# Optimization experiments

Hardware: AMD Instinct MI355X
Metric: run time of the kernel (lower is better)

Reference implementation:

```python
import jax, jax.numpy as jnp
import numpy as np

TOP_K = 2  # num_experts_per_tok


def setup_inputs() -> dict:
    key = jax.random.key(0)
    k1, k2, k3, k4, k5 = jax.random.split(key, 5)
    B, S, D, F, E = 2, 1024, 1024, 2048, 8
    return {
        "x": jax.random.normal(k1, (B, S, D), dtype=jnp.float32),
        "router_kernel_DE": jax.random.normal(k2, (D, E), dtype=jnp.float32) * 0.02,
        "kernel_gating_EDF": jax.random.normal(k3, (E, D, F), dtype=jnp.float32) * 0.02,
        "kernel_up_EDF": jax.random.normal(k4, (E, D, F), dtype=jnp.float32) * 0.02,
        "kernel_down_EFD": jax.random.normal(k5, (E, F, D), dtype=jnp.float32) * 0.02,
    }


def reference(x, router_kernel_DE, kernel_gating_EDF, kernel_up_EDF, kernel_down_EFD):
    E = router_kernel_DE.shape[-1]
    x = x.astype(jnp.float32)
    # --- Router ---
    logits_BSE = jnp.einsum('BSD,DE->BSE', x, router_kernel_DE)
    probs_BSE = jax.nn.softmax(logits_BSE.astype(jnp.float32), axis=-1)
    weights_BSK, indices_BSK = jax.lax.top_k(probs_BSE, TOP_K)
    norm_weights_BSK = jax.nn.softmax(weights_BSK, axis=-1)
    # scatter top-k weights into dense [B,S,E]
    one_hot_BSKE = jax.nn.one_hot(indices_BSK, num_classes=E, dtype=x.dtype)
    full_weights_BSE = jnp.sum(one_hot_BSKE * norm_weights_BSK[..., None], axis=2)
    # --- Dense-over-all-experts MoE forward ---
    gating_BSEF = jnp.einsum('BSD,EDF->BSEF', x, kernel_gating_EDF)
    act_BSEF = jax.nn.silu(gating_BSEF)
    up_BSEF = jnp.einsum('BSD,EDF->BSEF', x, kernel_up_EDF)
    fuse_BSEF = act_BSEF * up_BSEF
    down_BSED = jnp.einsum('BSEF,EFD->BSED', fuse_BSEF, kernel_down_EFD)
    out_BSD = jnp.einsum('BSED,BSE->BSD', down_BSED, full_weights_BSE)
    return out_BSD.astype(jnp.float32)
```

## Files before the change

### kernel.cpp

```cpp
#include <hip/hip_runtime.h>
#include <hip/hip_bf16.h>
#include <stdint.h>

#define T_TOK 2048
#define DIM 1024
#define FDIM 2048
#define NEXP 8
#define NSLOT 4096

typedef short bf16x8 __attribute__((ext_vector_type(8)));
typedef float f32x4 __attribute__((ext_vector_type(4)));

__device__ __forceinline__ unsigned short f2bf(float f) {
  union { float f; unsigned int u; } v; v.f = f;
  unsigned int r = v.u + 0x7FFFu + ((v.u >> 16) & 1u);
  return (unsigned short)(r >> 16);
}

__device__ __forceinline__ void gld_lds16(const void* g, void* l) {
  __builtin_amdgcn_global_load_lds(
      (const __attribute__((address_space(1))) unsigned int*)g,
      (__attribute__((address_space(3))) unsigned int*)l, 16, 0, 0);
}

__global__ void router_kernel(const float* __restrict__ x, const float* __restrict__ rk,
                              int* __restrict__ counts, int* __restrict__ tok_e,
                              float* __restrict__ tok_w) {
  int w = threadIdx.x >> 6, lane = threadIdx.x & 63;
  int t = blockIdx.x * 4 + w;
  float acc[NEXP];
#pragma unroll
  for (int e = 0; e < NEXP; ++e) acc[e] = 0.f;
  const float4* xr = (const float4*)(x + (size_t)t * DIM);
#pragma unroll
  for (int i = 0; i < 4; ++i) {
    float4 xv = xr[i * 64 + lane];
    int d0 = (i * 64 + lane) * 4;
#pragma unroll
    for (int j = 0; j < 4; ++j) {
      const float4* rr = (const float4*)(rk + (size_t)(d0 + j) * NEXP);
      float4 r0 = rr[0], r1 = rr[1];
      float xs = (j == 0) ? xv.x : (j == 1) ? xv.y : (j == 2) ? xv.z : xv.w;
      acc[0] += xs * r0.x; acc[1] += xs * r0.y; acc[2] += xs * r0.z; acc[3] += xs * r0.w;
      acc[4] += xs * r1.x; acc[5] += xs * r1.y; acc[6] += xs * r1.z; acc[7] += xs * r1.w;
    }
  }
#pragma unroll
  for (int off = 32; off > 0; off >>= 1) {
#pragma unroll
    for (int e = 0; e < NEXP; ++e) acc[e] += __shfl_xor(acc[e], off, 64);
  }
  if (lane == 0) {
    float m = acc[0];
    for (int e = 1; e < NEXP; ++e) m = fmaxf(m, acc[e]);
    float p[NEXP], s = 0.f;
    for (int e = 0; e < NEXP; ++e) { p[e] = expf(acc[e] - m); s += p[e]; }
    float inv = 1.f / s;
    for (int e = 0; e < NEXP; ++e) p[e] *= inv;
    int i1 = 0;
    for (int e = 1; e < NEXP; ++e) if (p[e] > p[i1]) i1 = e;
    int i2 = (i1 == 0) ? 1 : 0;
    for (int e = 0; e < NEXP; ++e) if (e != i1 && p[e] > p[i2]) i2 = e;
    float e1 = expf(p[i1]), e2 = expf(p[i2]);
    float winv = 1.f / (e1 + e2);
    tok_e[t * 2] = i1; tok_e[t * 2 + 1] = i2;
    tok_w[t * 2] = e1 * winv; tok_w[t * 2 + 1] = e2 * winv;
    atomicAdd(&counts[i1], 1); atomicAdd(&counts[i2], 1);
  }
}

__global__ void scan_kernel(const int* __restrict__ counts, int* __restrict__ offsets) {
  if (threadIdx.x == 0) {
    int s = 0;
    for (int e = 0; e < NEXP; ++e) { offsets[e] = s; s += counts[e]; }
  }
}

__global__ void assign_kernel(const int* __restrict__ tok_e, const float* __restrict__ tok_w,
                              const int* __restrict__ offsets, int* __restrict__ cursor,
                              int* __restrict__ slot_token, float* __restrict__ slot_weight,
                              int* __restrict__ tok_slot) {
  int t = blockIdx.x * 256 + threadIdx.x;
  if (t >= T_TOK) return;
#pragma unroll
  for (int k = 0; k < 2; ++k) {
    int e = tok_e[t * 2 + k];
    int pos = atomicAdd(&cursor[e], 1);
    int slot = offsets[e] + pos;
    slot_token[slot] = t;
    slot_weight[slot] = tok_w[t * 2 + k];
    tok_slot[t * 2 + k] = slot;
  }
}

__global__ void cvt_x_kernel(const float* __restrict__ x, unsigned short* __restrict__ xb) {
  int i = blockIdx.x * 256 + threadIdx.x;
  const float4* p = (const float4*)x;
  float4 a = p[i * 2], b = p[i * 2 + 1];
  uint4 o;
  o.x = ((unsigned)f2bf(a.y) << 16) | f2bf(a.x);
  o.y = ((unsigned)f2bf(a.w) << 16) | f2bf(a.z);
  o.z = ((unsigned)f2bf(b.y) << 16) | f2bf(b.x);
  o.w = ((unsigned)f2bf(b.w) << 16) | f2bf(b.z);
  ((uint4*)xb)[i] = o;
}

__global__ void transpose_cvt_kernel(const float* __restrict__ in, unsigned short* __restrict__ out,
                                     int R, int C) {
  __shared__ float lds[64][65];
  int e = blockIdx.z;
  size_t base = (size_t)e * (size_t)R * (size_t)C;
  int rb = blockIdx.y * 64, cb = blockIdx.x * 64;
  int tid = threadIdx.x;
  int col4 = (tid & 15) * 4, row = tid >> 4;
#pragma unroll
  for (int it = 0; it < 4; ++it) {
    int r = row + it * 16;
    float4 v = *(const float4*)(in + base + (size_t)(rb + r) * C + cb + col4);
    lds[col4 + 0][r] = v.x; lds[col4 + 1][r] = v.y;
    lds[col4 + 2][r] = v.z; lds[col4 + 3][r] = v.w;
  }
  __syncthreads();
  int r2 = (tid & 31) * 2, c = tid >> 5;
#pragma unroll
  for (int it = 0; it < 8; ++it) {
    int cc = c + it * 8;
    unsigned v = ((unsigned)f2bf(lds[cc][r2 + 1]) << 16) | f2bf(lds[cc][r2]);
    *(unsigned*)(out + base + (size_t)(cb + cc) * R + rb + r2) = v;
  }
}


__global__ __launch_bounds__(256) void gemm_gateup(
    const unsigned short* __restrict__ xb, const unsigned short* __restrict__ wg,
    const unsigned short* __restrict__ wu, const int* __restrict__ counts,
    const int* __restrict__ offsets, const int* __restrict__ slot_token,
    unsigned short* __restrict__ fuse) {
  int e = blockIdx.z;
  int cnt = counts[e];
  int mt = blockIdx.y;
  if (mt * 128 >= cnt) return;
  int off = offsets[e];
  int nt = blockIdx.x;
  __shared__ unsigned short Al[2][128 * 64];
  __shared__ unsigned short Bgl[2][128 * 64];
  __shared__ unsigned short Bul[2][128 * 64];
  int tid = threadIdx.x, w = tid >> 6, lane = tid & 63;
  int w4 = w * 4;
  int csrc = ((lane & 7) ^ (lane >> 3)) * 8;
  const unsigned short* asrc[4];
  const unsigned short* bgsrc[4];
  const unsigned short* busrc[4];
#pragma unroll
  for (int ii = 0; ii < 4; ++ii) {
    int i = w4 + ii;
    int r = i * 8 + (lane >> 3);
    int row = mt * 128 + r;
    int tok = (row < cnt) ? slot_token[off + row] : 0;
    asrc[ii] = xb + (size_t)tok * DIM + csrc;
    size_t frow = (size_t)e * FDIM + (size_t)(nt * 128 + r);
    bgsrc[ii] = wg + frow * DIM + csrc;
    busrc[ii] = wu + frow * DIM + csrc;
  }
  f32x4 accg[4][4] = {};
  f32x4 accu[4][4] = {};
  int wr = (w >> 1) * 64, wc = (w & 1) * 64;
  int swz = (lane & 7) << 3;
  int kof0 = ((lane >> 4) * 8) ^ swz;
  int kof1 = (32 + (lane >> 4) * 8) ^ swz;

  auto stage = [&](int buf, int k0) {
#pragma unroll
    for (int ii = 0; ii < 4; ++ii) {
      int i = w4 + ii;
      gld_lds16(asrc[ii] + k0, &Al[buf][i * 512]);
      gld_lds16(bgsrc[ii] + k0, &Bgl[buf][i * 512]);
      gld_lds16(busrc[ii] + k0, &Bul[buf][i * 512]);
    }
  };
  auto compute = [&](int buf) {
#pragma unroll
    for (int kk = 0; kk < 2; ++kk) {
      int kof = kk ? kof1 : kof0;
      bf16x8 af[4], bg[4], bu[4];
#pragma unroll
      for (int q = 0; q < 4; ++q) {
        af[q] = *(const bf16x8*)&Al[buf][(wr + q * 16 + (lane & 15)) * 64 + kof];
        bg[q] = *(const bf16x8*)&Bgl[buf][(wc + q * 16 + (lane & 15)) * 64 + kof];
        bu[q] = *(const bf16x8*)&Bul[buf][(wc + q * 16 + (lane & 15)) * 64 + kof];
      }
#pragma unroll
      for (int m4 = 0; m4 < 4; ++m4) {
#pragma unroll
        for (int n4 = 0; n4 < 4; ++n4) {
          accg[m4][n4] = __builtin_amdgcn_mfma_f32_16x16x32_bf16(af[m4], bg[n4], accg[m4][n4], 0, 0, 0);
          accu[m4][n4] = __builtin_amdgcn_mfma_f32_16x16x32_bf16(af[m4], bu[n4], accu[m4][n4], 0, 0, 0);
        }
      }
    }
  };

  stage(0, 0);
  __syncthreads();
#pragma unroll
  for (int k0 = 0; k0 < DIM; k0 += 128) {
    stage(1, k0 + 64);
    compute(0);
    __syncthreads();
    if (k0 + 128 < DIM) stage(0, k0 + 128);
    compute(1);
    __syncthreads();
  }

#pragma unroll
  for (int m4 = 0; m4 < 4; ++m4) {
#pragma unroll
    for (int n4 = 0; n4 < 4; ++n4) {
      f32x4 g = accg[m4][n4], u = accu[m4][n4];
#pragma unroll
      for (int j = 0; j < 4; ++j) {
        int r = wr + m4 * 16 + (lane >> 4) * 4 + j;
        int row = mt * 128 + r;
        if (row < cnt) {
          float gv = g[j];
          float val = gv / (1.f + expf(-gv)) * u[j];
          int f = nt * 128 + wc + n4 * 16 + (lane & 15);
          fuse[(size_t)(off + row) * FDIM + f] = f2bf(val);
        }
      }
    }
  }
}

__global__ __launch_bounds__(256) void gemm_down(
    const unsigned short* __restrict__ fuse, const unsigned short* __restrict__ wd,
    const int* __restrict__ counts, const int* __restrict__ offsets,
    const float* __restrict__ slot_weight, float* __restrict__ part) {
  int e = blockIdx.z;
  int cnt = counts[e];
  int mt = blockIdx.y;
  if (mt * 128 >= cnt) return;
  int off = offsets[e];
  int nt = blockIdx.x;
  __shared__ unsigned short Al[2][128 * 64];
  __shared__ unsigned short Bl[2][128 * 64];
  int tid = threadIdx.x, w = tid >> 6, lane = tid & 63;
  int w4 = w * 4;
  int csrc = ((lane & 7) ^ (lane >> 3)) * 8;
  const unsigned short* asrc[4];
  const unsigned short* bsrc[4];
#pragma unroll
  for (int ii = 0; ii < 4; ++ii) {
    int i = w4 + ii;
    int r = i * 8 + (lane >> 3);
    int row = mt * 128 + r;
    int grow = (row < cnt) ? (off + row) : off;
    asrc[ii] = fuse + (size_t)grow * FDIM + csrc;
    size_t drow = (size_t)e * DIM + (size_t)(nt * 128 + r);
    bsrc[ii] = wd + drow * FDIM + csrc;
  }
  f32x4 acc[4][4] = {};
  int wr = (w >> 1) * 64, wc = (w & 1) * 64;
  int swz = (lane & 7) << 3;
  int kof0 = ((lane >> 4) * 8) ^ swz;
  int kof1 = (32 + (lane >> 4) * 8) ^ swz;

  auto stage = [&](int buf, int k0) {
#pragma unroll
    for (int ii = 0; ii < 4; ++ii) {
      int i = w4 + ii;
      gld_lds16(asrc[ii] + k0, &Al[buf][i * 512]);
      gld_lds16(bsrc[ii] + k0, &Bl[buf][i * 512]);
    }
  };
  auto compute = [&](int buf) {
#pragma unroll
    for (int kk = 0; kk < 2; ++kk) {
      int kof = kk ? kof1 : kof0;
      bf16x8 af[4], bfr[4];
#pragma unroll
      for (int q = 0; q < 4; ++q) {
        af[q] = *(const bf16x8*)&Al[buf][(wr + q * 16 + (lane & 15)) * 64 + kof];
        bfr[q] = *(const bf16x8*)&Bl[buf][(wc + q * 16 + (lane & 15)) * 64 + kof];
      }
#pragma unroll
      for (int m4 = 0; m4 < 4; ++m4) {
#pragma unroll
        for (int n4 = 0; n4 < 4; ++n4) {
          acc[m4][n4] = __builtin_amdgcn_mfma_f32_16x16x32_bf16(af[m4], bfr[n4], acc[m4][n4], 0, 0, 0);
        }
      }
    }
  };

  stage(0, 0);
  __syncthreads();
#pragma unroll
  for (int k0 = 0; k0 < FDIM; k0 += 128) {
    stage(1, k0 + 64);
    compute(0);
    __syncthreads();
    if (k0 + 128 < FDIM) stage(0, k0 + 128);
    compute(1);
    __syncthreads();
  }

#pragma unroll
  for (int m4 = 0; m4 < 4; ++m4) {
#pragma unroll
    for (int j = 0; j < 4; ++j) {
      int r = wr + m4 * 16 + (lane >> 4) * 4 + j;
      int row = mt * 128 + r;
      if (row < cnt) {
        float wgt = slot_weight[off + row];
#pragma unroll
        for (int n4 = 0; n4 < 4; ++n4) {
          int d = nt * 128 + wc + n4 * 16 + (lane & 15);
          part[(size_t)(off + row) * DIM + d] = acc[m4][n4][j] * wgt;
        }
      }
    }
  }
}

__global__ void combine_kernel(const float* __restrict__ part, const int* __restrict__ tok_slot,
                               float* __restrict__ out) {
  int i = blockIdx.x * 256 + threadIdx.x;
  int t = i >> 8;
  int c = i & 255;
  int s0 = tok_slot[t * 2], s1 = tok_slot[t * 2 + 1];
  float4 a = ((const float4*)(part + (size_t)s0 * DIM))[c];
  float4 b = ((const float4*)(part + (size_t)s1 * DIM))[c];
  float4 o;
  o.x = a.x + b.x; o.y = a.y + b.y; o.z = a.z + b.z; o.w = a.w + b.w;
  ((float4*)(out + (size_t)t * DIM))[c] = o;
}

extern "C" void kernel_launch(void* const* d_in, const int* in_sizes, int n_in,
                              void* d_out, int out_size, void* d_ws, size_t ws_size,
                              hipStream_t stream) {
  (void)in_sizes; (void)n_in; (void)out_size;
  const float* x    = (const float*)d_in[0];
  const float* rk   = (const float*)d_in[1];
  const float* wg_f = (const float*)d_in[2];
  const float* wu_f = (const float*)d_in[3];
  const float* wd_f = (const float*)d_in[4];
  float* out = (float*)d_out;

  char* ws = (char*)d_ws;
  size_t o_xb   = 0;
  size_t o_wg   = o_xb + (size_t)T_TOK * DIM * 2;
  size_t o_wu   = o_wg + (size_t)NEXP * FDIM * DIM * 2;
  size_t o_wd   = o_wu + (size_t)NEXP * FDIM * DIM * 2;
  size_t o_fuse = o_wd + (size_t)NEXP * DIM * FDIM * 2;
  size_t o_part = o_fuse + (size_t)NSLOT * FDIM * 2;
  size_t o_meta = o_part + (size_t)NSLOT * DIM * 4;
  size_t o_counts = o_meta;
  size_t o_cursor = o_counts + 32;
  size_t o_offs   = o_cursor + 32;
  size_t o_tok_e  = o_offs + 32;
  size_t o_tok_w  = o_tok_e + (size_t)T_TOK * 2 * 4;
  size_t o_tok_s  = o_tok_w + (size_t)T_TOK * 2 * 4;
  size_t o_st     = o_tok_s + (size_t)T_TOK * 2 * 4;
  size_t o_sw     = o_st + (size_t)NSLOT * 4;
  size_t need     = o_sw + (size_t)NSLOT * 4;
  if (ws_size < need) return;

  unsigned short* xb   = (unsigned short*)(ws + o_xb);
  unsigned short* wgt  = (unsigned short*)(ws + o_wg);
  unsigned short* wut  = (unsigned short*)(ws + o_wu);
  unsigned short* wdt  = (unsigned short*)(ws + o_wd);
  unsigned short* fuse = (unsigned short*)(ws + o_fuse);
  float* part          = (float*)(ws + o_part);
  int* counts          = (int*)(ws + o_counts);
  int* cursor          = (int*)(ws + o_cursor);
  int* offsets         = (int*)(ws + o_offs);
  int* tok_e           = (int*)(ws + o_tok_e);
  float* tok_w         = (float*)(ws + o_tok_w);
  int* tok_slot        = (int*)(ws + o_tok_s);
  int* slot_token      = (int*)(ws + o_st);
  float* slot_weight   = (float*)(ws + o_sw);

  hipMemsetAsync(ws + o_counts, 0, 64, stream);
  router_kernel<<<T_TOK / 4, 256, 0, stream>>>(x, rk, counts, tok_e, tok_w);
  scan_kernel<<<1, 64, 0, stream>>>(counts, offsets);
  assign_kernel<<<T_TOK / 256, 256, 0, stream>>>(tok_e, tok_w, offsets, cursor,
                                                 slot_token, slot_weight, tok_slot);
  cvt_x_kernel<<<(T_TOK * DIM / 8) / 256, 256, 0, stream>>>(x, xb);
  transpose_cvt_kernel<<<dim3(FDIM / 64, DIM / 64, NEXP), 256, 0, stream>>>(wg_f, wgt, DIM, FDIM);
  transpose_cvt_kernel<<<dim3(FDIM / 64, DIM / 64, NEXP), 256, 0, stream>>>(wu_f, wut, DIM, FDIM);
  transpose_cvt_kernel<<<dim3(DIM / 64, FDIM / 64, NEXP), 256, 0, stream>>>(wd_f, wdt, FDIM, DIM);
  gemm_gateup<<<dim3(FDIM / 128, 16, NEXP), 256, 0, stream>>>(xb, wgt, wut, counts, offsets,
                                                              slot_token, fuse);
  gemm_down<<<dim3(DIM / 128, 16, NEXP), 256, 0, stream>>>(fuse, wdt, counts, offsets,
                                                           slot_weight, part);
  combine_kernel<<<(T_TOK * DIM / 4) / 256, 256, 0, stream>>>(part, tok_slot, out);
}
```

Measured before the change: 293.9 us.

## Use partial vmcnt waits to overlap next-tile loads with MFMA compute

Rewrites the K loops of both the gate/up and down GEMM kernels as a rolled double-buffer pipeline. Each iteration issues the async global-to-LDS loads for the next tile, waits only for the older loads with a partial s_waitcnt vmcnt, then runs the MFMAs on the current buffer. The goal is to stop draining all outstanding loads at every __syncthreads so memory traffic overlaps compute. It relies on hand-counted vmcnt values (12 and 8) matching the number of loads each stage issues; a wrong count would let compute read incomplete LDS data.

```diff
diff --git a/kernel.cpp b/kernel.cpp
--- a/kernel.cpp
+++ b/kernel.cpp
@@ -201,16 +201,21 @@
   };
 
   stage(0, 0);
-  __syncthreads();
-#pragma unroll
-  for (int k0 = 0; k0 < DIM; k0 += 128) {
-    stage(1, k0 + 64);
-    compute(0);
-    __syncthreads();
-    if (k0 + 128 < DIM) stage(0, k0 + 128);
-    compute(1);
-    __syncthreads();
-  }
+  int cb = 0;
+  for (int k0 = 0; k0 < DIM - 64; k0 += 64) {
+    stage(cb ^ 1, k0 + 64);
+    asm volatile("s_waitcnt vmcnt(12)" ::: "memory");
+    __builtin_amdgcn_s_barrier();
+    __builtin_amdgcn_sched_barrier(0);
+    compute(cb);
+    __builtin_amdgcn_sched_barrier(0);
+    __builtin_amdgcn_s_barrier();
+    cb ^= 1;
+  }
+  asm volatile("s_waitcnt vmcnt(0)" ::: "memory");
+  __builtin_amdgcn_s_barrier();
+  __builtin_amdgcn_sched_barrier(0);
+  compute(cb);
 
 #pragma unroll
   for (int m4 = 0; m4 < 4; ++m4) {
@@ -294,16 +299,21 @@
   };
 
   stage(0, 0);
-  __syncthreads();
-#pragma unroll
-  for (int k0 = 0; k0 < FDIM; k0 += 128) {
-    stage(1, k0 + 64);
-    compute(0);
-    __syncthreads();
-    if (k0 + 128 < FDIM) stage(0, k0 + 128);
-    compute(1);
-    __syncthreads();
-  }
+  int cb = 0;
+  for (int k0 = 0; k0 < FDIM - 64; k0 += 64) {
+    stage(cb ^ 1, k0 + 64);
+    asm volatile("s_waitcnt vmcnt(8)" ::: "memory");
+    __builtin_amdgcn_s_barrier();
+    __builtin_amdgcn_sched_barrier(0);
+    compute(cb);
+    __builtin_amdgcn_sched_barrier(0);
+    __builtin_amdgcn_s_barrier();
+    cb ^= 1;
+  }
+  asm volatile("s_waitcnt vmcnt(0)" ::: "memory");
+  __builtin_amdgcn_s_barrier();
+  __builtin_amdgcn_sched_barrier(0);
+  compute(cb);
 
 #pragma unroll
   for (int m4 = 0; m4 < 4; ++m4) {
```

After: 294.8 us. Within noise of the previous version (+0.3%).
